# Optimization experiments

Measured on AMD Instinct MI355X. Metric: run time of the kernel, lower is better.

The kernel has to match this reference:

```python
import jax, jax.numpy as jnp
import numpy as np

D_MODEL = 1024
N_HEADS = 8
D_KEYS = D_MODEL // N_HEADS  # 128
D_LLM = 4096


def setup_inputs() -> dict:
    key = jax.random.key(0)
    ks = jax.random.split(key, 11)
    Bm, Lq, Vs = 8, 1024, 2048
    inner = D_KEYS * N_HEADS  # 1024
    s = 0.02
    return {
        "Q": jax.random.normal(ks[0], (Bm, Lq, D_MODEL), jnp.float32),
        "K_src": jax.random.normal(ks[1], (Vs, D_LLM), jnp.float32),
        "V_src": jax.random.normal(ks[2], (Vs, D_LLM), jnp.float32),
        "Wq": jax.random.normal(ks[3], (D_MODEL, inner), jnp.float32) * s,
        "bq": jnp.zeros((inner,), jnp.float32),
        "Wk": jax.random.normal(ks[4], (D_LLM, inner), jnp.float32) * s,
        "bk": jnp.zeros((inner,), jnp.float32),
        "Wv": jax.random.normal(ks[5], (D_LLM, inner), jnp.float32) * s,
        "bv": jnp.zeros((inner,), jnp.float32),
        "Wo": jax.random.normal(ks[6], (inner, D_LLM), jnp.float32) * s,
        "bo": jnp.zeros((D_LLM,), jnp.float32),
    }


def reference(Q, K_src, V_src, Wq, bq, Wk, bk, Wv, bv, Wo, bo):
    Bm, Lq, _ = Q.shape
    Vs, d_llm = K_src.shape
    H = N_HEADS
    Ek = d_llm // H  # NOTE: torch code scales by d_llm//H, not d_keys
    q = (Q @ Wq + bq).reshape(Bm, Lq, H, -1)           # [B,Lq,H,E]
    k = (K_src @ Wk + bk).reshape(Vs, H, -1)            # [S,H,E]
    v = (V_src @ Wv + bv).reshape(Vs, H, -1)            # [S,H,E]
    scale = 1.0 / jnp.sqrt(jnp.asarray(Ek, q.dtype))
    scores = jnp.einsum("blhe,she->bhls", q, k)         # [B,H,Lq,S]
    A = jax.nn.softmax(scale * scores, axis=-1)         # dropout = identity (eval)
    out = jnp.einsum("bhls,she->blhe", A, v)            # [B,Lq,H,E]
    out = out.reshape(Bm, Lq, -1)
    return out @ Wo + bo                                 # [B,Lq,d_llm]
```

## Files before the change

### kernel.cpp

```cpp
#include <hip/hip_runtime.h>
#include <hip/hip_bf16.h>


typedef __bf16 bf16x8 __attribute__((ext_vector_type(8)));
typedef float  f32x4  __attribute__((ext_vector_type(4)));

union V16 { uint4 u; bf16x8 v; };
__device__ __forceinline__ bf16x8 ld16v(const void* p) {
  V16 t; t.u = *(const uint4*)p; return t.v;
}
__device__ __forceinline__ uint4 pack8(float4 a, float4 b) {
  V16 t;
  t.v[0] = (__bf16)a.x; t.v[1] = (__bf16)a.y; t.v[2] = (__bf16)a.z; t.v[3] = (__bf16)a.w;
  t.v[4] = (__bf16)b.x; t.v[5] = (__bf16)b.y; t.v[6] = (__bf16)b.z; t.v[7] = (__bf16)b.w;
  return t.u;
}

__global__ __launch_bounds__(256) void transpose_k(const float* __restrict__ W,
                                                   __bf16* __restrict__ Wt, int K, int N) {
  __shared__ __bf16 t[32][33];
  int tx = threadIdx.x & 31, ty = threadIdx.x >> 5;
  int n0 = blockIdx.x * 32, k0 = blockIdx.y * 32;
#pragma unroll
  for (int r = 0; r < 32; r += 8) t[ty + r][tx] = (__bf16)W[(size_t)(k0 + ty + r) * N + n0 + tx];
  __syncthreads();
#pragma unroll
  for (int r = 0; r < 32; r += 8) Wt[(size_t)(n0 + ty + r) * K + k0 + tx] = t[tx][ty + r];
}

template <typename AT, typename CT>
__device__ __forceinline__ void gemm_core(__bf16 (*As)[40], __bf16 (*Bs)[40],
                                          const AT* __restrict__ A,
                                          const __bf16* __restrict__ Bt,
                                          const float* __restrict__ bias,
                                          CT* __restrict__ C,
                                          int M, int N, int K, int lda, int trans,
                                          int m0, int n0) {
  const int tid = threadIdx.x;
  const int lane = tid & 63, wave = tid >> 6;
  const int g = lane >> 4, l16 = lane & 15;
  const int wr = wave >> 1, wc = wave & 1;
  f32x4 acc[4][4] = {};
  for (int k0 = 0; k0 < K; k0 += 32) {
    __syncthreads();
#pragma unroll
    for (int i = 0; i < 2; i++) {
      int c = tid + i * 256;
      int row = c >> 2, col = (c & 3) * 8;
      if constexpr (sizeof(AT) == 4) {
        const float* ap = (const float*)A + (size_t)(m0 + row) * lda + k0 + col;
        float4 f0 = *(const float4*)ap;
        float4 f1 = *(const float4*)(ap + 4);
        *(uint4*)&As[row][col] = pack8(f0, f1);
      } else {
        *(uint4*)&As[row][col] = *(const uint4*)((const __bf16*)A + (size_t)(m0 + row) * lda + k0 + col);
      }
      *(uint4*)&Bs[row][col] = *(const uint4*)(Bt + (size_t)(n0 + row) * (size_t)K + k0 + col);
    }
    __syncthreads();
    bf16x8 af[4], bff[4];
#pragma unroll
    for (int mf = 0; mf < 4; mf++) af[mf]  = ld16v(&As[wr * 64 + mf * 16 + l16][g * 8]);
#pragma unroll
    for (int nf = 0; nf < 4; nf++) bff[nf] = ld16v(&Bs[wc * 64 + nf * 16 + l16][g * 8]);
#pragma unroll
    for (int mf = 0; mf < 4; mf++)
#pragma unroll
      for (int nf = 0; nf < 4; nf++)
        acc[mf][nf] = __builtin_amdgcn_mfma_f32_16x16x32_bf16(af[mf], bff[nf], acc[mf][nf], 0, 0, 0);
  }
#pragma unroll
  for (int nf = 0; nf < 4; nf++) {
    int col = n0 + wc * 64 + nf * 16 + l16;
    float bv = bias[col];
#pragma unroll
    for (int mf = 0; mf < 4; mf++) {
      int rowb = m0 + wr * 64 + mf * 16 + g * 4;
      if constexpr (sizeof(CT) == 2) {
        if (trans) {
          union { __bf16 h[4]; uint2 u; } pk;
#pragma unroll
          for (int r = 0; r < 4; r++) pk.h[r] = (__bf16)(acc[mf][nf][r] + bv);
          *(uint2*)&((__bf16*)C)[(size_t)col * M + rowb] = pk.u;
        } else {
#pragma unroll
          for (int r = 0; r < 4; r++)
            ((__bf16*)C)[(size_t)(rowb + r) * N + col] = (__bf16)(acc[mf][nf][r] + bv);
        }
      } else {
#pragma unroll
        for (int r = 0; r < 4; r++)
          ((float*)C)[(size_t)(rowb + r) * N + col] = acc[mf][nf][r] + bv;
      }
    }
  }
}

__global__ __launch_bounds__(256) void gemm_f_b(const float* __restrict__ A,
                                                const __bf16* __restrict__ Bt,
                                                const float* __restrict__ bias,
                                                __bf16* __restrict__ C,
                                                int M, int N, int K, int lda, int trans) {
  __shared__ __bf16 As[128][40];
  __shared__ __bf16 Bs[128][40];
  gemm_core<float, __bf16>(As, Bs, A, Bt, bias, C, M, N, K, lda, trans,
                           blockIdx.x * 128, blockIdx.y * 128);
}

__global__ __launch_bounds__(256) void gemm_b_f(const __bf16* __restrict__ A,
                                                const __bf16* __restrict__ Bt,
                                                const float* __restrict__ bias,
                                                float* __restrict__ C,
                                                int M, int N, int K, int lda, int trans) {
  __shared__ __bf16 As[128][40];
  __shared__ __bf16 Bs[128][40];
  gemm_core<__bf16, float>(As, Bs, A, Bt, bias, C, M, N, K, lda, trans,
                           blockIdx.x * 128, blockIdx.y * 128);
}

__global__ __launch_bounds__(256) void gemm_kv(const float* __restrict__ A0, const __bf16* __restrict__ B0t,
                                               const float* __restrict__ b0, __bf16* __restrict__ C0,
                                               const float* __restrict__ A1, const __bf16* __restrict__ B1t,
                                               const float* __restrict__ b1, __bf16* __restrict__ C1) {
  __shared__ __bf16 As[128][40];
  __shared__ __bf16 Bs[128][40];
  if (blockIdx.z == 0)
    gemm_core<float, __bf16>(As, Bs, A0, B0t, b0, C0, 2048, 1024, 4096, 4096, 0,
                             blockIdx.x * 128, blockIdx.y * 128);
  else
    gemm_core<float, __bf16>(As, Bs, A1, B1t, b1, C1, 2048, 1024, 4096, 4096, 1,
                             blockIdx.x * 128, blockIdx.y * 128);
}

__global__ __launch_bounds__(256) void attn_k(const __bf16* __restrict__ q,
                                              const __bf16* __restrict__ k,
                                              const __bf16* __restrict__ vt,
                                              __bf16* __restrict__ o) {
  __shared__ __bf16 ks[64][136];
  __shared__ __bf16 vs[128][72];
  __shared__ __bf16 ps[128][72];
  const int tid = threadIdx.x, lane = tid & 63, wave = tid >> 6;
  const int g = lane >> 4, l16 = lane & 15;
  const int h = blockIdx.y, q0 = blockIdx.x * 128;
  const float scale = 0.044194173824159216f;

  bf16x8 qf[2][4];
#pragma unroll
  for (int mf = 0; mf < 2; mf++)
#pragma unroll
    for (int kk = 0; kk < 4; kk++) {
      int row = q0 + wave * 32 + mf * 16 + l16;
      qf[mf][kk] = ld16v(q + (size_t)row * 1024 + h * 128 + kk * 32 + g * 8);
    }

  f32x4 accO[2][8] = {};
  float m_i[2][4], l_i[2][4];
#pragma unroll
  for (int a = 0; a < 2; a++)
#pragma unroll
    for (int b = 0; b < 4; b++) { m_i[a][b] = -1e30f; l_i[a][b] = 0.f; }

  for (int s0 = 0; s0 < 2048; s0 += 64) {
    __syncthreads();
#pragma unroll
    for (int i = 0; i < 4; i++) {
      int c = tid + i * 256;
      { int row = c >> 4, col = (c & 15) * 8;
        *(uint4*)&ks[row][col] = *(const uint4*)(k + (size_t)(s0 + row) * 1024 + h * 128 + col); }
      { int row = c >> 3, col = (c & 7) * 8;
        *(uint4*)&vs[row][col] = *(const uint4*)(vt + (size_t)(h * 128 + row) * 2048 + s0 + col); }
    }
    __syncthreads();

    f32x4 sc[2][4] = {};
#pragma unroll
    for (int kk = 0; kk < 4; kk++) {
      bf16x8 kf[4];
#pragma unroll
      for (int nf = 0; nf < 4; nf++) kf[nf] = ld16v(&ks[nf * 16 + l16][kk * 32 + g * 8]);
#pragma unroll
      for (int mf = 0; mf < 2; mf++)
#pragma unroll
        for (int nf = 0; nf < 4; nf++)
          sc[mf][nf] = __builtin_amdgcn_mfma_f32_16x16x32_bf16(qf[mf][kk], kf[nf], sc[mf][nf], 0, 0, 0);
    }
#pragma unroll
    for (int mf = 0; mf < 2; mf++)
#pragma unroll
      for (int nf = 0; nf < 4; nf++) sc[mf][nf] *= scale;

#pragma unroll
    for (int mf = 0; mf < 2; mf++)
#pragma unroll
      for (int r = 0; r < 4; r++) {
        float mx = fmaxf(fmaxf(sc[mf][0][r], sc[mf][1][r]), fmaxf(sc[mf][2][r], sc[mf][3][r]));
#pragma unroll
        for (int off = 1; off < 16; off <<= 1) mx = fmaxf(mx, __shfl_xor(mx, off));
        float mo = m_i[mf][r];
        float mn = fmaxf(mo, mx);
        float alpha = __expf(mo - mn);
        float rs = 0.f;
#pragma unroll
        for (int nf = 0; nf < 4; nf++) {
          float p = __expf(sc[mf][nf][r] - mn);
          sc[mf][nf][r] = p;
          rs += p;
        }
#pragma unroll
        for (int off = 1; off < 16; off <<= 1) rs += __shfl_xor(rs, off);
        m_i[mf][r] = mn;
        l_i[mf][r] = l_i[mf][r] * alpha + rs;
#pragma unroll
        for (int ef = 0; ef < 8; ef++) accO[mf][ef][r] *= alpha;
        int prow = wave * 32 + mf * 16 + g * 4 + r;
#pragma unroll
        for (int nf = 0; nf < 4; nf++) ps[prow][nf * 16 + l16] = (__bf16)sc[mf][nf][r];
      }

    __syncthreads();

#pragma unroll
    for (int kk = 0; kk < 2; kk++) {
      bf16x8 pf[2];
#pragma unroll
      for (int mf = 0; mf < 2; mf++) pf[mf] = ld16v(&ps[wave * 32 + mf * 16 + l16][kk * 32 + g * 8]);
#pragma unroll
      for (int ef = 0; ef < 8; ef++) {
        bf16x8 vf = ld16v(&vs[ef * 16 + l16][kk * 32 + g * 8]);
#pragma unroll
        for (int mf = 0; mf < 2; mf++)
          accO[mf][ef] = __builtin_amdgcn_mfma_f32_16x16x32_bf16(pf[mf], vf, accO[mf][ef], 0, 0, 0);
      }
    }
  }

#pragma unroll
  for (int mf = 0; mf < 2; mf++)
#pragma unroll
    for (int ef = 0; ef < 8; ef++)
#pragma unroll
      for (int r = 0; r < 4; r++) {
        int row = q0 + wave * 32 + mf * 16 + g * 4 + r;
        int col = h * 128 + ef * 16 + l16;
        o[(size_t)row * 1024 + col] = (__bf16)(accO[mf][ef][r] / l_i[mf][r]);
      }
}

extern "C" void kernel_launch(void* const* d_in, const int* in_sizes, int n_in,
                              void* d_out, int out_size, void* d_ws, size_t ws_size,
                              hipStream_t stream) {
  const float* Q   = (const float*)d_in[0];
  const float* Ksr = (const float*)d_in[1];
  const float* Vsr = (const float*)d_in[2];
  const float* Wq  = (const float*)d_in[3];
  const float* bq  = (const float*)d_in[4];
  const float* Wk  = (const float*)d_in[5];
  const float* bk  = (const float*)d_in[6];
  const float* Wv  = (const float*)d_in[7];
  const float* bv  = (const float*)d_in[8];
  const float* Wo  = (const float*)d_in[9];
  const float* bo  = (const float*)d_in[10];
  __bf16* ws = (__bf16*)d_ws;
  const size_t MB = 1024 * 1024;
  __bf16* qb  = ws;
  __bf16* kb  = ws + 8  * MB;
  __bf16* vtb = ws + 10 * MB;
  __bf16* at  = ws + 12 * MB;
  __bf16* WqT = ws + 20 * MB;
  __bf16* WkT = ws + 21 * MB;
  __bf16* WvT = ws + 25 * MB;
  __bf16* WoT = ws + 29 * MB;

  transpose_k<<<dim3(32, 32),  256, 0, stream>>>(Wq, WqT, 1024, 1024);
  transpose_k<<<dim3(32, 128), 256, 0, stream>>>(Wk, WkT, 4096, 1024);
  transpose_k<<<dim3(32, 128), 256, 0, stream>>>(Wv, WvT, 4096, 1024);
  transpose_k<<<dim3(128, 32), 256, 0, stream>>>(Wo, WoT, 1024, 4096);

  gemm_f_b<<<dim3(64, 8), 256, 0, stream>>>(Q, WqT, bq, qb, 8192, 1024, 1024, 1024, 0);
  gemm_kv<<<dim3(16, 8, 2), 256, 0, stream>>>(Ksr, WkT, bk, kb, Vsr, WvT, bv, vtb);
  attn_k<<<dim3(64, 8), 256, 0, stream>>>(qb, kb, vtb, at);
  gemm_b_f<<<dim3(64, 32), 256, 0, stream>>>(at, WoT, bo, (float*)d_out, 8192, 4096, 1024, 1024, 0);
}
```

Baseline: 732.2 us.

## Use direct global-to-LDS loads with XOR swizzle in GEMMs; alias attention K/P LDS

In the GEMM core, the bf16 operand tiles are now loaded with global_load_lds direct-to-LDS transfers instead of going through registers. The padded [128][40] tiles become unpadded 128x32 tiles with an XOR swizzle on 16-byte chunks, chosen to avoid bank conflicts on the fragment reads. In the attention kernel, the K tile and the P tile share one LDS union, and the P write is moved after the barrier, so per-block LDS shrinks and more blocks can be resident. The risks are DMA completion and wait ordering, and the fp32 A path still converting through registers.

```diff
diff --git a/kernel.cpp b/kernel.cpp
--- a/kernel.cpp
+++ b/kernel.cpp
@@ -15,6 +15,14 @@
   t.v[4] = (__bf16)b.x; t.v[5] = (__bf16)b.y; t.v[6] = (__bf16)b.z; t.v[7] = (__bf16)b.w;
   return t.u;
 }
+__device__ __forceinline__ void dma16(const void* g, void* l) {
+  __builtin_amdgcn_global_load_lds(
+      (const __attribute__((address_space(1))) unsigned int*)g,
+      (__attribute__((address_space(3))) unsigned int*)l, 16, 0, 0);
+}
+__device__ __forceinline__ int chunk_of(int row, int gc) {
+  return row * 4 + (gc ^ ((row >> 1) & 3));
+}
 
 __global__ __launch_bounds__(256) void transpose_k(const float* __restrict__ W,
                                                    __bf16* __restrict__ Wt, int K, int N) {
@@ -29,7 +37,7 @@
 }
 
 template <typename AT, typename CT>
-__device__ __forceinline__ void gemm_core(__bf16 (*As)[40], __bf16 (*Bs)[40],
+__device__ __forceinline__ void gemm_core(__bf16* As, __bf16* Bs,
                                           const AT* __restrict__ A,
                                           const __bf16* __restrict__ Bt,
                                           const float* __restrict__ bias,
@@ -40,29 +48,49 @@
   const int lane = tid & 63, wave = tid >> 6;
   const int g = lane >> 4, l16 = lane & 15;
   const int wr = wave >> 1, wc = wave & 1;
+  int aoff[4], boff[4];
+#pragma unroll
+  for (int mf = 0; mf < 4; mf++) aoff[mf] = chunk_of(wr * 64 + mf * 16 + l16, g) * 8;
+#pragma unroll
+  for (int nf = 0; nf < 4; nf++) boff[nf] = chunk_of(wc * 64 + nf * 16 + l16, g) * 8;
+
   f32x4 acc[4][4] = {};
   for (int k0 = 0; k0 < K; k0 += 32) {
     __syncthreads();
-#pragma unroll
-    for (int i = 0; i < 2; i++) {
-      int c = tid + i * 256;
-      int row = c >> 2, col = (c & 3) * 8;
-      if constexpr (sizeof(AT) == 4) {
-        const float* ap = (const float*)A + (size_t)(m0 + row) * lda + k0 + col;
+    if constexpr (sizeof(AT) == 2) {
+#pragma unroll
+      for (int rnd = 0; rnd < 2; rnd++) {
+        int cstart = wave * 128 + rnd * 64;
+        int p = cstart + lane;
+        int row = p >> 2, gc = (p & 3) ^ ((row >> 1) & 3);
+        dma16((const __bf16*)A + (size_t)(m0 + row) * lda + k0 + gc * 8,
+              As + (size_t)cstart * 8);
+      }
+    } else {
+#pragma unroll
+      for (int i = 0; i < 2; i++) {
+        int p = tid + i * 256;
+        int row = p >> 2, gc = (p & 3) ^ ((row >> 1) & 3);
+        const float* ap = (const float*)A + (size_t)(m0 + row) * lda + k0 + gc * 8;
         float4 f0 = *(const float4*)ap;
         float4 f1 = *(const float4*)(ap + 4);
-        *(uint4*)&As[row][col] = pack8(f0, f1);
-      } else {
-        *(uint4*)&As[row][col] = *(const uint4*)((const __bf16*)A + (size_t)(m0 + row) * lda + k0 + col);
-      }
-      *(uint4*)&Bs[row][col] = *(const uint4*)(Bt + (size_t)(n0 + row) * (size_t)K + k0 + col);
+        *(uint4*)(As + p * 8) = pack8(f0, f1);
+      }
+    }
+#pragma unroll
+    for (int rnd = 0; rnd < 2; rnd++) {
+      int cstart = wave * 128 + rnd * 64;
+      int p = cstart + lane;
+      int row = p >> 2, gc = (p & 3) ^ ((row >> 1) & 3);
+      dma16(Bt + (size_t)(n0 + row) * (size_t)K + k0 + gc * 8,
+            Bs + (size_t)cstart * 8);
     }
     __syncthreads();
     bf16x8 af[4], bff[4];
 #pragma unroll
-    for (int mf = 0; mf < 4; mf++) af[mf]  = ld16v(&As[wr * 64 + mf * 16 + l16][g * 8]);
-#pragma unroll
-    for (int nf = 0; nf < 4; nf++) bff[nf] = ld16v(&Bs[wc * 64 + nf * 16 + l16][g * 8]);
+    for (int mf = 0; mf < 4; mf++) af[mf]  = ld16v(As + aoff[mf]);
+#pragma unroll
+    for (int nf = 0; nf < 4; nf++) bff[nf] = ld16v(Bs + boff[nf]);
 #pragma unroll
     for (int mf = 0; mf < 4; mf++)
 #pragma unroll
@@ -101,8 +129,8 @@
                                                 const float* __restrict__ bias,
                                                 __bf16* __restrict__ C,
                                                 int M, int N, int K, int lda, int trans) {
-  __shared__ __bf16 As[128][40];
-  __shared__ __bf16 Bs[128][40];
+  __shared__ __align__(16) __bf16 As[128 * 32];
+  __shared__ __align__(16) __bf16 Bs[128 * 32];
   gemm_core<float, __bf16>(As, Bs, A, Bt, bias, C, M, N, K, lda, trans,
                            blockIdx.x * 128, blockIdx.y * 128);
 }
@@ -112,8 +140,8 @@
                                                 const float* __restrict__ bias,
                                                 float* __restrict__ C,
                                                 int M, int N, int K, int lda, int trans) {
-  __shared__ __bf16 As[128][40];
-  __shared__ __bf16 Bs[128][40];
+  __shared__ __align__(16) __bf16 As[128 * 32];
+  __shared__ __align__(16) __bf16 Bs[128 * 32];
   gemm_core<__bf16, float>(As, Bs, A, Bt, bias, C, M, N, K, lda, trans,
                            blockIdx.x * 128, blockIdx.y * 128);
 }
@@ -122,8 +150,8 @@
                                                const float* __restrict__ b0, __bf16* __restrict__ C0,
                                                const float* __restrict__ A1, const __bf16* __restrict__ B1t,
                                                const float* __restrict__ b1, __bf16* __restrict__ C1) {
-  __shared__ __bf16 As[128][40];
-  __shared__ __bf16 Bs[128][40];
+  __shared__ __align__(16) __bf16 As[128 * 32];
+  __shared__ __align__(16) __bf16 Bs[128 * 32];
   if (blockIdx.z == 0)
     gemm_core<float, __bf16>(As, Bs, A0, B0t, b0, C0, 2048, 1024, 4096, 4096, 0,
                              blockIdx.x * 128, blockIdx.y * 128);
@@ -136,9 +164,11 @@
                                               const __bf16* __restrict__ k,
                                               const __bf16* __restrict__ vt,
                                               __bf16* __restrict__ o) {
-  __shared__ __bf16 ks[64][136];
+  __shared__ union {
+    __bf16 ks[64][136];
+    __bf16 ps[128][72];
+  } u;
   __shared__ __bf16 vs[128][72];
-  __shared__ __bf16 ps[128][72];
   const int tid = threadIdx.x, lane = tid & 63, wave = tid >> 6;
   const int g = lane >> 4, l16 = lane & 15;
   const int h = blockIdx.y, q0 = blockIdx.x * 128;
@@ -166,7 +196,7 @@
     for (int i = 0; i < 4; i++) {
       int c = tid + i * 256;
       { int row = c >> 4, col = (c & 15) * 8;
-        *(uint4*)&ks[row][col] = *(const uint4*)(k + (size_t)(s0 + row) * 1024 + h * 128 + col); }
+        *(uint4*)&u.ks[row][col] = *(const uint4*)(k + (size_t)(s0 + row) * 1024 + h * 128 + col); }
       { int row = c >> 3, col = (c & 7) * 8;
         *(uint4*)&vs[row][col] = *(const uint4*)(vt + (size_t)(h * 128 + row) * 2048 + s0 + col); }
     }
@@ -177,7 +207,7 @@
     for (int kk = 0; kk < 4; kk++) {
       bf16x8 kf[4];
 #pragma unroll
-      for (int nf = 0; nf < 4; nf++) kf[nf] = ld16v(&ks[nf * 16 + l16][kk * 32 + g * 8]);
+      for (int nf = 0; nf < 4; nf++) kf[nf] = ld16v(&u.ks[nf * 16 + l16][kk * 32 + g * 8]);
 #pragma unroll
       for (int mf = 0; mf < 2; mf++)
 #pragma unroll
@@ -212,18 +242,24 @@
         l_i[mf][r] = l_i[mf][r] * alpha + rs;
 #pragma unroll
         for (int ef = 0; ef < 8; ef++) accO[mf][ef][r] *= alpha;
+      }
+
+    __syncthreads();
+
+#pragma unroll
+    for (int mf = 0; mf < 2; mf++)
+#pragma unroll
+      for (int r = 0; r < 4; r++) {
         int prow = wave * 32 + mf * 16 + g * 4 + r;
 #pragma unroll
-        for (int nf = 0; nf < 4; nf++) ps[prow][nf * 16 + l16] = (__bf16)sc[mf][nf][r];
-      }
-
-    __syncthreads();
+        for (int nf = 0; nf < 4; nf++) u.ps[prow][nf * 16 + l16] = (__bf16)sc[mf][nf][r];
+      }
 
 #pragma unroll
     for (int kk = 0; kk < 2; kk++) {
       bf16x8 pf[2];
 #pragma unroll
-      for (int mf = 0; mf < 2; mf++) pf[mf] = ld16v(&ps[wave * 32 + mf * 16 + l16][kk * 32 + g * 8]);
+      for (int mf = 0; mf < 2; mf++) pf[mf] = ld16v(&u.ps[wave * 32 + mf * 16 + l16][kk * 32 + g * 8]);
 #pragma unroll
       for (int ef = 0; ef < 8; ef++) {
         bf16x8 vf = ld16v(&vs[ef * 16 + l16][kk * 32 + g * 8]);
```

New measurement: 721.0 us. No clear change (-1.5%).
